# Performance work log

Measured on AMD Instinct MI355X. Metric: run time of the kernel, lower is better.

## Reference

```python
import jax, jax.numpy as jnp
import numpy as np

CH = 8        # CHANNELS
CONVS = 8     # CONVOLUTIONS
HID = 32      # HIDDEN
NTYPES = 6    # NODE_TYPES
N_NODES = 200000
N_EDGES = 6400000
ENTRIES = 2048
BN_EPS = 1e-5


def setup_inputs() -> dict:
    key = jax.random.key(0)
    ks = jax.random.split(key, 12)
    x = jax.random.randint(ks[0], (N_NODES,), 0, NTYPES)
    edge_index = jax.random.randint(ks[1], (2, N_EDGES), 0, N_NODES)
    entry_index = jax.random.randint(ks[2], (ENTRIES,), 0, N_NODES)
    emb = jax.random.normal(ks[3], (NTYPES, CH), jnp.float32)
    bn_gamma = jnp.ones((CONVS, CH), jnp.float32)
    bn_beta = jnp.zeros((CONVS, CH), jnp.float32)
    conv_w = jax.random.normal(ks[4], (CONVS, CH, CH), jnp.float32) * (1.0 / np.sqrt(CH))
    conv_b = jnp.zeros((CONVS, CH), jnp.float32)
    hidden_w = jax.random.normal(ks[5], (2 * CH, HID), jnp.float32) * (1.0 / np.sqrt(2 * CH))
    hidden_b = jnp.zeros((HID,), jnp.float32)
    out_w = jax.random.normal(ks[6], (HID, 1), jnp.float32) * (1.0 / np.sqrt(HID))
    out_b = jnp.zeros((1,), jnp.float32)
    return dict(x=x, edge_index=edge_index, entry_index=entry_index, emb=emb,
                bn_gamma=bn_gamma, bn_beta=bn_beta, conv_w=conv_w, conv_b=conv_b,
                hidden_w=hidden_w, hidden_b=hidden_b, out_w=out_w, out_b=out_b)


def reference(x, edge_index, entry_index, emb, bn_gamma, bn_beta,
              conv_w, conv_b, hidden_w, hidden_b, out_w, out_b):
    N = x.shape[0]
    src, dst = edge_index[0], edge_index[1]
    # GCN symmetric normalization with self-loops (PyG gcn_norm):
    # deg[i] = 1 (self loop) + in-degree(i); norm_e = deg[src]^-1/2 * deg[dst]^-1/2
    deg = jax.ops.segment_sum(jnp.ones(src.shape[0], jnp.float32), dst, num_segments=N) + 1.0
    dinv = jax.lax.rsqrt(deg)                       # [N]
    enorm = (dinv[src] * dinv[dst])[:, None]        # [E,1]
    self_norm = (dinv * dinv)[:, None]              # [N,1] self-loop coefficient

    h = emb[x]                                      # [N,CH]
    for l in range(CONVS):
        # BatchNorm (training mode: batch statistics over nodes)
        mu = h.mean(axis=0)
        var = jnp.mean((h - mu) ** 2, axis=0)
        hn = (h - mu) * jax.lax.rsqrt(var + BN_EPS) * bn_gamma[l] + bn_beta[l]
        # GCNConv: linear transform then normalized aggregation
        ht = hn @ conv_w[l]                         # [N,CH]
        agg = jax.ops.segment_sum(ht[src] * enorm, dst, num_segments=N)
        agg = agg + ht * self_norm + conv_b[l]
        h = jax.nn.relu(h + agg)                    # residual + ReLU

    xe = h[entry_index]                             # [E,CH]
    E = xe.shape[0]
    # cartesian_prod(line, line): pair[i,j] = concat(xe[i], xe[j])
    pair = jnp.concatenate([
        jnp.broadcast_to(xe[:, None, :], (E, E, CH)),
        jnp.broadcast_to(xe[None, :, :], (E, E, CH)),
    ], axis=-1)                                     # [E,E,2CH]
    hid = jax.nn.relu(pair @ hidden_w + hidden_b)   # [E,E,HID]
    out = (hid @ out_w + out_b).reshape(E, E)
    return out
```

## Files before the change

kernel.cpp:

```cpp
#include <hip/hip_runtime.h>
#include <hip/hip_fp16.h>

#define NNODES 200000
#define NEDGES 6400000
#define NENT   2048
#define CH     8
#define HID    32
#define NCONV  8
#define BN_EPS 1e-5f

#define BSZ    512
#define NBUCK  ((NNODES + BSZ - 1) / BSZ)
#define HB     (NBUCK/2)
#define CHUNK  4096
#define NCHUNK ((NEDGES + CHUNK - 1) / CHUNK)
#define SPAD   16
#define SUBCAP 12288

#define FXSCALE   2097152.0f
#define FXINV     (1.0f/2097152.0f)

__global__ __launch_bounds__(256) void k_chist(const int* __restrict__ dst, int* __restrict__ cnt, int E){
  __shared__ int hist[NBUCK];
  for(int t=threadIdx.x; t<NBUCK; t+=256) hist[t]=0;
  __syncthreads();
  int e0 = blockIdx.x*CHUNK;
  int n = min(CHUNK, E-e0);
  for(int i=threadIdx.x; i<n; i+=256) atomicAdd(&hist[dst[e0+i]>>9], 1);
  __syncthreads();
  for(int t=threadIdx.x; t<NBUCK; t+=256) cnt[(size_t)blockIdx.x*NBUCK + t] = hist[t];
}

__global__ __launch_bounds__(256) void k_cscan(int* __restrict__ cnt, int* __restrict__ total){
  int b = blockIdx.x;
  __shared__ int sd[256];
  int carry = 0;
  for(int base=0; base<NCHUNK; base+=256){
    int c = base + threadIdx.x;
    int v = (c<NCHUNK) ? cnt[(size_t)c*NBUCK + b] : 0;
    sd[threadIdx.x] = v; __syncthreads();
    #pragma unroll
    for(int o=1; o<256; o<<=1){
      int x = (threadIdx.x>=o) ? sd[threadIdx.x-o] : 0;
      __syncthreads();
      sd[threadIdx.x] += x;
      __syncthreads();
    }
    if(c<NCHUNK) cnt[(size_t)c*NBUCK + b] = carry + sd[threadIdx.x] - v;
    carry += sd[255];
    __syncthreads();
  }
  if(threadIdx.x==0) total[b] = carry;
}

__global__ __launch_bounds__(512) void k_bscan(const int* __restrict__ total, int* __restrict__ bbase){
  __shared__ int sd[512];
  int t = threadIdx.x;
  int v = (t<NBUCK) ? total[t] : 0;
  sd[t] = v; __syncthreads();
  #pragma unroll
  for(int o=1; o<512; o<<=1){
    int x = (t>=o) ? sd[t-o] : 0;
    __syncthreads();
    sd[t] += x;
    __syncthreads();
  }
  if(t<NBUCK) bbase[t] = sd[t] - v;
  if(t==511) bbase[NBUCK] = sd[511];
}

__global__ __launch_bounds__(512) void k_bin(const int* __restrict__ src, const int* __restrict__ dst,
                                             const int* __restrict__ cnt, const int* __restrict__ bbase,
                                             unsigned int* __restrict__ binned, int E){
  __shared__ int hist[NBUCK], excl[NBUCK], cur[NBUCK], base[NBUCK];
  __shared__ unsigned int pin[CHUNK];
  __shared__ unsigned short bk_in[CHUNK];
  __shared__ unsigned int sorted[CHUNK];
  __shared__ unsigned short sbkt[CHUNK];
  __shared__ int sd[512];
  int c = blockIdx.x;
  int e0 = c*CHUNK, n = min(CHUNK, E-e0);
  for(int t=threadIdx.x; t<NBUCK; t+=512) hist[t]=0;
  __syncthreads();
  for(int i=threadIdx.x; i<n; i+=512){
    int s = src[e0+i], d = dst[e0+i];
    int b = d>>9;
    pin[i]   = ((unsigned)(d & (BSZ-1))<<18) | (unsigned)s;
    bk_in[i] = (unsigned short)b;
    atomicAdd(&hist[b], 1);
  }
  __syncthreads();
  int t = threadIdx.x;
  int hv = (t<NBUCK) ? hist[t] : 0;
  sd[t] = hv; __syncthreads();
  #pragma unroll
  for(int o=1; o<512; o<<=1){
    int x = (t>=o) ? sd[t-o] : 0;
    __syncthreads();
    sd[t] += x;
    __syncthreads();
  }
  if(t<NBUCK){
    int ex = sd[t] - hv;
    excl[t] = ex; cur[t] = ex;
    base[t] = bbase[t] + cnt[(size_t)c*NBUCK + t];
  }
  __syncthreads();
  for(int i=threadIdx.x; i<n; i+=512){
    int b = bk_in[i];
    int slot = atomicAdd(&cur[b], 1);
    sorted[slot] = pin[i];
    sbkt[slot]   = (unsigned short)b;
  }
  __syncthreads();
  for(int i=threadIdx.x; i<n; i+=512){
    int b = sbkt[i];
    binned[ base[b] + (i - excl[b]) ] = sorted[i];
  }
}

__global__ __launch_bounds__(512) void k_sub(const unsigned int* __restrict__ binned,
                                             const int* __restrict__ bbase,
                                             unsigned int* __restrict__ binned2,
                                             float* __restrict__ dinv, int N){
  __shared__ int hd[BSZ];
  __shared__ int hs[NBUCK];
  __shared__ int cur[NBUCK];
  __shared__ int sd[512];
  __shared__ int hbase_s;
  __shared__ unsigned int stage[SUBCAP];
  int b = blockIdx.x >> 1, half = blockIdx.x & 1;
  int t = threadIdx.x;
  hd[t] = 0;
  if(t < NBUCK) hs[t] = 0;
  __syncthreads();
  int s0 = bbase[b], s1 = bbase[b+1];
  if(half == 0){
    for(int i=s0+t; i<s1; i+=512){
      unsigned p = binned[i];
      atomicAdd(&hd[p>>18], 1);
      atomicAdd(&hs[(p & 0x3FFFF)>>9], 1);
    }
  } else {
    for(int i=s0+t; i<s1; i+=512){
      unsigned p = binned[i];
      atomicAdd(&hs[(p & 0x3FFFF)>>9], 1);
    }
  }
  __syncthreads();
  if(half == 0){
    int node = b*BSZ + t;
    if(node < N) dinv[node] = 1.0f / sqrtf((float)hd[t] + 1.0f);
  }
  int hv = (t<NBUCK) ? hs[t] : 0;
  sd[t] = hv; __syncthreads();
  #pragma unroll
  for(int o=1; o<512; o<<=1){
    int x = (t>=o) ? sd[t-o] : 0;
    __syncthreads();
    sd[t] += x;
    __syncthreads();
  }
  int ex = sd[t] - hv;
  if(t == HB) hbase_s = ex;
  __syncthreads();
  int lo = half ? hbase_s : 0;
  int hi = half ? (s1 - s0) : hbase_s;
  if(t < NBUCK) cur[t] = ex - lo;
  __syncthreads();
  int len = hi - lo;
  if(len <= SUBCAP){
    for(int i=s0+t; i<s1; i+=512){
      unsigned p = binned[i];
      int bin = (p & 0x3FFFF)>>9;
      bool mine = half ? (bin >= HB) : (bin < HB);
      if(mine){
        int slot = atomicAdd(&cur[bin], 1);
        stage[slot] = p;
      }
    }
    __syncthreads();
    for(int i=t; i<len; i+=512) binned2[s0 + lo + i] = stage[i];
  } else {
    for(int i=s0+t; i<s1; i+=512){
      unsigned p = binned[i];
      int bin = (p & 0x3FFFF)>>9;
      bool mine = half ? (bin >= HB) : (bin < HB);
      if(mine){
        int slot = atomicAdd(&cur[bin], 1);
        binned2[s0 + lo + slot] = p;
      }
    }
  }
}

__global__ __launch_bounds__(256) void k_init_h(const int* __restrict__ x, const float* __restrict__ emb,
                                                float* __restrict__ h, float* __restrict__ stats0, int N){
  int i = blockIdx.x*256 + threadIdx.x;
  float v[CH];
  #pragma unroll
  for(int c=0;c<CH;c++) v[c]=0.f;
  if(i < N){
    int tt = x[i];
    const float4* ep = (const float4*)(emb + (size_t)tt*CH);
    float4 a = ep[0], b = ep[1];
    float4* hp = (float4*)(h + (size_t)i*CH);
    hp[0] = a; hp[1] = b;
    v[0]=a.x; v[1]=a.y; v[2]=a.z; v[3]=a.w; v[4]=b.x; v[5]=b.y; v[6]=b.z; v[7]=b.w;
  }
  float s[CH], q[CH];
  #pragma unroll
  for(int c=0;c<CH;c++){ s[c]=v[c]; q[c]=v[c]*v[c]; }
  #pragma unroll
  for(int off=32; off>0; off>>=1){
    #pragma unroll
    for(int c=0;c<CH;c++){ s[c]+=__shfl_down(s[c],off); q[c]+=__shfl_down(q[c],off); }
  }
  __shared__ float ls[4][2*CH];
  int wave = threadIdx.x>>6, lane = threadIdx.x&63;
  if(lane==0){
    #pragma unroll
    for(int c=0;c<CH;c++){ ls[wave][c]=s[c]; ls[wave][CH+c]=q[c]; }
  }
  __syncthreads();
  if(threadIdx.x < 2*CH){
    float tsum = ls[0][threadIdx.x]+ls[1][threadIdx.x]+ls[2][threadIdx.x]+ls[3][threadIdx.x];
    unsafeAtomicAdd(&stats0[threadIdx.x*SPAD], tsum);
  }
}

__global__ __launch_bounds__(256) void k_ht(const float* __restrict__ h, const float* __restrict__ stats_l,
                                            const float* __restrict__ gamma, const float* __restrict__ beta,
                                            const float* __restrict__ convw,
                                            const float* __restrict__ dinv,
                                            __half* __restrict__ hts16, int l, int N){
  __shared__ float A[CH*CH], c0[CH], sA[CH], sT[CH];
  int t = threadIdx.x;
  if(t < CH){
    const float invN = 1.0f / (float)NNODES;
    float mu  = stats_l[t*SPAD]      * invN;
    float ex2 = stats_l[(CH+t)*SPAD] * invN;
    float var = ex2 - mu*mu;
    float r   = 1.0f / sqrtf(var + BN_EPS);
    float sc  = r * gamma[l*CH+t];
    sA[t] = sc;
    sT[t] = beta[l*CH+t] - mu*sc;
  }
  __syncthreads();
  if(t < CH*CH){
    int ci = t>>3, co = t&7;
    A[t] = sA[ci] * convw[(l*CH+ci)*CH+co];
  }
  if(t < CH){
    float a = 0.f;
    #pragma unroll
    for(int ci=0;ci<CH;ci++) a += sT[ci]*convw[(l*CH+ci)*CH+t];
    c0[t] = a;
  }
  __syncthreads();
  int i = blockIdx.x*blockDim.x + threadIdx.x;
  if(i >= N) return;
  const float4* hp = (const float4*)(h + (size_t)i*CH);
  float4 a = hp[0], b = hp[1];
  float v[CH] = {a.x,a.y,a.z,a.w,b.x,b.y,b.z,b.w};
  float o[CH];
  #pragma unroll
  for(int co=0;co<CH;co++) o[co]=c0[co];
  #pragma unroll
  for(int ci=0;ci<CH;ci++){
    float vv = v[ci];
    #pragma unroll
    for(int co=0;co<CH;co++) o[co] += vv*A[ci*CH+co];
  }
  float dn = dinv[i];
  union { __half hh[CH]; uint4 u; } pk;
  #pragma unroll
  for(int c=0;c<CH;c++) pk.hh[c] = __float2half(o[c]*dn);
  *(uint4*)(hts16 + (size_t)i*CH) = pk.u;
}

__global__ __launch_bounds__(1024) void k_push(const unsigned int* __restrict__ binned2,
                                               const int* __restrict__ bbase,
                                               const __half* __restrict__ hts16,
                                               const float* __restrict__ dinv,
                                               const float* __restrict__ convb,
                                               float* __restrict__ h, float* __restrict__ stats_next,
                                               int l, int N){
  __shared__ int acc[BSZ*CH];
  int b = blockIdx.x, t = threadIdx.x;
  for(int i=t; i<BSZ*CH; i+=1024) acc[i] = 0;
  __syncthreads();
  int s0 = bbase[b], s1 = bbase[b+1];
  int lane8 = t & 7;
  int g = t >> 3;
  for(int base = s0 + g*4; base < s1; base += 512){
    int m = s1 - base;
    if(m >= 4){
      unsigned p0 = binned2[base], p1 = binned2[base+1], p2 = binned2[base+2], p3 = binned2[base+3];
      float v0 = __half2float(hts16[(size_t)(p0 & 0x3FFFF)*CH + lane8]);
      float v1 = __half2float(hts16[(size_t)(p1 & 0x3FFFF)*CH + lane8]);
      float v2 = __half2float(hts16[(size_t)(p2 & 0x3FFFF)*CH + lane8]);
      float v3 = __half2float(hts16[(size_t)(p3 & 0x3FFFF)*CH + lane8]);
      atomicAdd(&acc[(p0>>18)*CH + lane8], __float2int_rn(v0*FXSCALE));
      atomicAdd(&acc[(p1>>18)*CH + lane8], __float2int_rn(v1*FXSCALE));
      atomicAdd(&acc[(p2>>18)*CH + lane8], __float2int_rn(v2*FXSCALE));
      atomicAdd(&acc[(p3>>18)*CH + lane8], __float2int_rn(v3*FXSCALE));
    } else {
      for(int i=0; i<m; i++){
        unsigned p = binned2[base+i];
        float v = __half2float(hts16[(size_t)(p & 0x3FFFF)*CH + lane8]);
        atomicAdd(&acc[(p>>18)*CH + lane8], __float2int_rn(v*FXSCALE));
      }
    }
  }
  __syncthreads();
  float vv[CH];
  #pragma unroll
  for(int c=0;c<CH;c++) vv[c]=0.f;
  int node = b*BSZ + t;
  if(t < BSZ && node < N){
    const int4* ar = (const int4*)(acc + t*CH);
    int4 a0 = ar[0], a1 = ar[1];
    float av[CH] = {(float)a0.x*FXINV,(float)a0.y*FXINV,(float)a0.z*FXINV,(float)a0.w*FXINV,
                    (float)a1.x*FXINV,(float)a1.y*FXINV,(float)a1.z*FXINV,(float)a1.w*FXINV};
    uint4 su = *(const uint4*)(hts16 + (size_t)node*CH);
    const __half2* sp = (const __half2*)&su;
    float sv[CH];
    #pragma unroll
    for(int j=0;j<4;j++){
      float2 f = __half22float2(sp[j]);
      sv[2*j] = f.x; sv[2*j+1] = f.y;
    }
    const float4* hp = (const float4*)(h + (size_t)node*CH);
    float4 h0 = hp[0], h1 = hp[1];
    float hv2[CH] = {h0.x,h0.y,h0.z,h0.w,h1.x,h1.y,h1.z,h1.w};
    float dn = dinv[node];
    #pragma unroll
    for(int c=0;c<CH;c++){
      float r = hv2[c] + convb[l*CH + c] + dn*(av[c] + sv[c]);
      vv[c] = fmaxf(r, 0.f);
    }
    float4* hw4 = (float4*)(h + (size_t)node*CH);
    hw4[0] = make_float4(vv[0],vv[1],vv[2],vv[3]);
    hw4[1] = make_float4(vv[4],vv[5],vv[6],vv[7]);
  }
  float s[CH], q[CH];
  #pragma unroll
  for(int c=0;c<CH;c++){ s[c]=vv[c]; q[c]=vv[c]*vv[c]; }
  #pragma unroll
  for(int off=32; off>0; off>>=1){
    #pragma unroll
    for(int c=0;c<CH;c++){ s[c]+=__shfl_down(s[c],off); q[c]+=__shfl_down(q[c],off); }
  }
  __shared__ float ls[16][2*CH];
  int wave = t>>6, lane = t&63;
  if(lane==0){
    #pragma unroll
    for(int c=0;c<CH;c++){ ls[wave][c]=s[c]; ls[wave][CH+c]=q[c]; }
  }
  __syncthreads();
  if(t < 2*CH){
    float tot = 0.f;
    #pragma unroll
    for(int w=0; w<16; w++) tot += ls[w][t];
    unsafeAtomicAdd(&stats_next[t*SPAD], tot);
  }
}

__global__ __launch_bounds__(256) void k_uv(const int* __restrict__ entry, const float* __restrict__ h,
                                            const float* __restrict__ hw, const float* __restrict__ hb,
                                            float* __restrict__ u, float* __restrict__ v){
  __shared__ float w[2*CH*HID];
  __shared__ float b[HID];
  for(int t=threadIdx.x; t<2*CH*HID; t+=256) w[t]=hw[t];
  if(threadIdx.x<HID) b[threadIdx.x]=hb[threadIdx.x];
  __syncthreads();
  int k = blockIdx.x*blockDim.x + threadIdx.x;
  if(k >= NENT) return;
  int node = entry[k];
  const float4* hp = (const float4*)(h + (size_t)node*CH);
  float4 a = hp[0], b4 = hp[1];
  float xe[CH] = {a.x,a.y,a.z,a.w,b4.x,b4.y,b4.z,b4.w};
  #pragma unroll 4
  for(int c=0;c<HID;c++){
    float uu = 0.f, vv = b[c];
    #pragma unroll
    for(int ci=0;ci<CH;ci++){
      uu += xe[ci]*w[ci*HID+c];
      vv += xe[ci]*w[(CH+ci)*HID+c];
    }
    u[(size_t)k*HID+c] = uu;
    v[(size_t)k*HID+c] = vv;
  }
}

__global__ __launch_bounds__(256) void k_pair(const float* __restrict__ u, const float* __restrict__ v,
                                              const float* __restrict__ ow, const float* __restrict__ ob,
                                              float* __restrict__ out){
  __shared__ float us[16][HID+1];
  __shared__ float vs[64][HID+1];
  __shared__ float wo[HID];
  int tid = threadIdx.x;
  int jb = blockIdx.x*64, ib = blockIdx.y*16;
  for(int t=tid; t<16*HID; t+=256) us[t>>5][t&31] = u[(size_t)(ib + (t>>5))*HID + (t&31)];
  for(int t=tid; t<64*HID; t+=256) vs[t>>5][t&31] = v[(size_t)(jb + (t>>5))*HID + (t&31)];
  if(tid<HID) wo[tid]=ow[tid];
  __syncthreads();
  int tx = tid&63, ty = tid>>6;
  float a0=0.f, a1=0.f, a2=0.f, a3=0.f;
  #pragma unroll
  for(int c=0;c<HID;c++){
    float vv = vs[tx][c];
    float w  = wo[c];
    a0 += fmaxf(us[ty   ][c]+vv, 0.f)*w;
    a1 += fmaxf(us[ty+4 ][c]+vv, 0.f)*w;
    a2 += fmaxf(us[ty+8 ][c]+vv, 0.f)*w;
    a3 += fmaxf(us[ty+12][c]+vv, 0.f)*w;
  }
  float o0 = ob[0];
  size_t base = (size_t)ib*2048 + jb + tx;
  out[base + (size_t)(ty   )*2048] = a0+o0;
  out[base + (size_t)(ty+4 )*2048] = a1+o0;
  out[base + (size_t)(ty+8 )*2048] = a2+o0;
  out[base + (size_t)(ty+12)*2048] = a3+o0;
}

extern "C" void kernel_launch(void* const* d_in, const int* in_sizes, int n_in,
                              void* d_out, int out_size, void* d_ws, size_t ws_size,
                              hipStream_t stream){
  const int*   x     = (const int*)d_in[0];
  const int*   ei    = (const int*)d_in[1];
  const int*   entry = (const int*)d_in[2];
  const float* emb   = (const float*)d_in[3];
  const float* gamma = (const float*)d_in[4];
  const float* beta  = (const float*)d_in[5];
  const float* convw = (const float*)d_in[6];
  const float* convb = (const float*)d_in[7];
  const float* hw    = (const float*)d_in[8];
  const float* hb    = (const float*)d_in[9];
  const float* ow    = (const float*)d_in[10];
  const float* ob    = (const float*)d_in[11];
  const int* srcp = ei;
  const int* dstp = ei + NEDGES;

  char* ws = (char*)d_ws;
  size_t o = 0;
  auto alloc = [&](size_t bytes){ void* p = ws + o; o += (bytes + 255) & ~(size_t)255; return p; };
  int*      cnt    = (int*)     alloc((size_t)NCHUNK*NBUCK*4);
  int*      total  = (int*)     alloc(NBUCK*4);
  int*      bbase  = (int*)     alloc((NBUCK+1)*4);
  unsigned* binned = (unsigned*)alloc((size_t)NEDGES*4);
  unsigned* binned2= (unsigned*)alloc((size_t)NEDGES*4);
  float*    dinv   = (float*)   alloc(NNODES*4);
  float*    h      = (float*)   alloc((size_t)NNODES*CH*4);
  __half*   hts16  = (__half*)  alloc((size_t)NNODES*CH*2);
  float*    stats  = (float*)   alloc((NCONV+1)*2*CH*SPAD*4);
  float*    ub     = (float*)   alloc((size_t)NENT*HID*4);
  float*    vb     = (float*)   alloc((size_t)NENT*HID*4);
  (void)ws_size; (void)in_sizes; (void)n_in; (void)out_size;

  k_chist<<<NCHUNK, 256, 0, stream>>>(dstp, cnt, NEDGES);
  k_cscan<<<NBUCK, 256, 0, stream>>>(cnt, total);
  k_bscan<<<1, 512, 0, stream>>>(total, bbase);
  k_bin  <<<NCHUNK, 512, 0, stream>>>(srcp, dstp, cnt, bbase, binned, NEDGES);
  k_sub  <<<NBUCK*2, 512, 0, stream>>>(binned, bbase, binned2, dinv, NNODES);

  hipMemsetAsync(stats, 0, (NCONV+1)*2*CH*SPAD*sizeof(float), stream);
  k_init_h<<<(NNODES+255)/256, 256, 0, stream>>>(x, emb, h, stats, NNODES);

  for(int l=0; l<NCONV; l++){
    k_ht  <<<(NNODES+255)/256, 256, 0, stream>>>(h, stats + (size_t)l*2*CH*SPAD, gamma, beta, convw,
                                                 dinv, hts16, l, NNODES);
    k_push<<<NBUCK, 1024, 0, stream>>>(binned2, bbase, hts16, dinv, convb, h,
                                       stats + (size_t)(l+1)*2*CH*SPAD, l, NNODES);
  }

  k_uv<<<NENT/256, 256, 0, stream>>>(entry, h, hw, hb, ub, vb);
  dim3 pg(2048/64, 2048/16);
  k_pair<<<pg, 256, 0, stream>>>(ub, vb, ow, ob, (float*)d_out);
}
```

Before: 560.7 us.

## Split push blocks into half-edge-range blocks with global partial accumulators and finalize kernel

```diff
diff --git a/kernel.cpp b/kernel.cpp
--- a/kernel.cpp
+++ b/kernel.cpp
@@ -279,22 +279,24 @@
   *(uint4*)(hts16 + (size_t)i*CH) = pk.u;
 }
 
-__global__ __launch_bounds__(1024) void k_push(const unsigned int* __restrict__ binned2,
-                                               const int* __restrict__ bbase,
-                                               const __half* __restrict__ hts16,
-                                               const float* __restrict__ dinv,
-                                               const float* __restrict__ convb,
-                                               float* __restrict__ h, float* __restrict__ stats_next,
-                                               int l, int N){
+__global__ __launch_bounds__(512) void k_push(const unsigned int* __restrict__ binned2,
+                                              const int* __restrict__ bbase,
+                                              const __half* __restrict__ hts16,
+                                              int* __restrict__ pacc){
   __shared__ int acc[BSZ*CH];
-  int b = blockIdx.x, t = threadIdx.x;
-  for(int i=t; i<BSZ*CH; i+=1024) acc[i] = 0;
+  int bh = blockIdx.x, b = bh>>1, half = bh&1;
+  int t = threadIdx.x;
+  #pragma unroll
+  for(int i=t; i<BSZ*CH; i+=512) acc[i] = 0;
   __syncthreads();
   int s0 = bbase[b], s1 = bbase[b+1];
+  int mid = s0 + ((s1 - s0) >> 1);
+  int a0 = half ? mid : s0;
+  int a1 = half ? s1  : mid;
   int lane8 = t & 7;
   int g = t >> 3;
-  for(int base = s0 + g*4; base < s1; base += 512){
-    int m = s1 - base;
+  for(int base = a0 + g*4; base < a1; base += 256){
+    int m = a1 - base;
     if(m >= 4){
       unsigned p0 = binned2[base], p1 = binned2[base+1], p2 = binned2[base+2], p3 = binned2[base+3];
       float v0 = __half2float(hts16[(size_t)(p0 & 0x3FFFF)*CH + lane8]);
@@ -314,56 +316,45 @@
     }
   }
   __syncthreads();
-  float vv[CH];
-  #pragma unroll
-  for(int c=0;c<CH;c++) vv[c]=0.f;
-  int node = b*BSZ + t;
-  if(t < BSZ && node < N){
-    const int4* ar = (const int4*)(acc + t*CH);
-    int4 a0 = ar[0], a1 = ar[1];
-    float av[CH] = {(float)a0.x*FXINV,(float)a0.y*FXINV,(float)a0.z*FXINV,(float)a0.w*FXINV,
-                    (float)a1.x*FXINV,(float)a1.y*FXINV,(float)a1.z*FXINV,(float)a1.w*FXINV};
-    uint4 su = *(const uint4*)(hts16 + (size_t)node*CH);
-    const __half2* sp = (const __half2*)&su;
-    float sv[CH];
-    #pragma unroll
-    for(int j=0;j<4;j++){
-      float2 f = __half22float2(sp[j]);
-      sv[2*j] = f.x; sv[2*j+1] = f.y;
-    }
-    const float4* hp = (const float4*)(h + (size_t)node*CH);
-    float4 h0 = hp[0], h1 = hp[1];
-    float hv2[CH] = {h0.x,h0.y,h0.z,h0.w,h1.x,h1.y,h1.z,h1.w};
-    float dn = dinv[node];
-    #pragma unroll
-    for(int c=0;c<CH;c++){
-      float r = hv2[c] + convb[l*CH + c] + dn*(av[c] + sv[c]);
-      vv[c] = fmaxf(r, 0.f);
-    }
-    float4* hw4 = (float4*)(h + (size_t)node*CH);
-    hw4[0] = make_float4(vv[0],vv[1],vv[2],vv[3]);
-    hw4[1] = make_float4(vv[4],vv[5],vv[6],vv[7]);
-  }
-  float s[CH], q[CH];
-  #pragma unroll
-  for(int c=0;c<CH;c++){ s[c]=vv[c]; q[c]=vv[c]*vv[c]; }
-  #pragma unroll
-  for(int off=32; off>0; off>>=1){
-    #pragma unroll
-    for(int c=0;c<CH;c++){ s[c]+=__shfl_down(s[c],off); q[c]+=__shfl_down(q[c],off); }
-  }
-  __shared__ float ls[16][2*CH];
-  int wave = t>>6, lane = t&63;
-  if(lane==0){
-    #pragma unroll
-    for(int c=0;c<CH;c++){ ls[wave][c]=s[c]; ls[wave][CH+c]=q[c]; }
-  }
-  __syncthreads();
-  if(t < 2*CH){
-    float tot = 0.f;
-    #pragma unroll
-    for(int w=0; w<16; w++) tot += ls[w][t];
-    unsafeAtomicAdd(&stats_next[t*SPAD], tot);
+  int4* dst = (int4*)(pacc + (size_t)bh*BSZ*CH);
+  const int4* src = (const int4*)acc;
+  dst[t]       = src[t];
+  dst[t + 512] = src[t + 512];
+}
+
+__global__ __launch_bounds__(256) void k_fin(const int* __restrict__ pacc,
+                                             const __half* __restrict__ hts16,
+                                             const float* __restrict__ dinv,
+                                             const float* __restrict__ convb,
+                                             float* __restrict__ h, float* __restrict__ stats_next,
+                                             int l, int N){
+  int tid = blockIdx.x*256 + threadIdx.x;
+  int lane8 = tid & 7;
+  int node = tid >> 3;
+  float val = 0.f;
+  if(node < N){
+    int b  = node >> 9;
+    int dl = node & (BSZ-1);
+    int a0 = pacc[((size_t)(2*b  )*BSZ + dl)*CH + lane8];
+    int a1 = pacc[((size_t)(2*b+1)*BSZ + dl)*CH + lane8];
+    float a = (float)(a0 + a1) * FXINV;
+    float sv = __half2float(hts16[(size_t)node*CH + lane8]);
+    float hv = h[(size_t)node*CH + lane8];
+    float r = hv + convb[l*CH + lane8] + dinv[node]*(a + sv);
+    val = fmaxf(r, 0.f);
+    h[(size_t)node*CH + lane8] = val;
+  }
+  float S = val, Q = val*val;
+  S += __shfl_xor(S, 8);  Q += __shfl_xor(Q, 8);
+  S += __shfl_xor(S, 16); Q += __shfl_xor(Q, 16);
+  S += __shfl_xor(S, 32); Q += __shfl_xor(Q, 32);
+  __shared__ float ls[4][2*CH];
+  int wave = threadIdx.x>>6, wl = threadIdx.x&63;
+  if(wl < CH){ ls[wave][wl] = S; ls[wave][CH+wl] = Q; }
+  __syncthreads();
+  if(threadIdx.x < 2*CH){
+    float tsum = ls[0][threadIdx.x]+ls[1][threadIdx.x]+ls[2][threadIdx.x]+ls[3][threadIdx.x];
+    unsafeAtomicAdd(&stats_next[threadIdx.x*SPAD], tsum);
   }
 }
 
@@ -457,6 +448,7 @@
   float*    stats  = (float*)   alloc((NCONV+1)*2*CH*SPAD*4);
   float*    ub     = (float*)   alloc((size_t)NENT*HID*4);
   float*    vb     = (float*)   alloc((size_t)NENT*HID*4);
+  int*      pacc   = (int*)binned;
   (void)ws_size; (void)in_sizes; (void)n_in; (void)out_size;
 
   k_chist<<<NCHUNK, 256, 0, stream>>>(dstp, cnt, NEDGES);
@@ -471,8 +463,9 @@
   for(int l=0; l<NCONV; l++){
     k_ht  <<<(NNODES+255)/256, 256, 0, stream>>>(h, stats + (size_t)l*2*CH*SPAD, gamma, beta, convw,
                                                  dinv, hts16, l, NNODES);
-    k_push<<<NBUCK, 1024, 0, stream>>>(binned2, bbase, hts16, dinv, convb, h,
-                                       stats + (size_t)(l+1)*2*CH*SPAD, l, NNODES);
+    k_push<<<NBUCK*2, 512, 0, stream>>>(binned2, bbase, hts16, pacc);
+    k_fin <<<(NNODES*CH+255)/256, 256, 0, stream>>>(pacc, hts16, dinv, convb, h,
+                                                    stats + (size_t)(l+1)*2*CH*SPAD, l, NNODES);
   }
 
   k_uv<<<NENT/256, 256, 0, stream>>>(entry, h, hw, hb, ub, vb);
```

Result: slower. 1.700 ms (+203.1%).
